# Optimization experiments

Hardware: AMD Instinct MI355X
Metric: run time of the kernel (lower is better)

The kernel has to match this reference:

```python
import jax, jax.numpy as jnp
import numpy as np

N_HEADS = 16


def setup_inputs() -> dict:
    key = jax.random.key(0)
    k1, k2, k3, k4, k5 = jax.random.split(key, 5)
    B, T, C = 2, 2048, 1024
    x = jax.random.normal(k1, (B, T, C), dtype=jnp.float32)
    rotary_cos_sin = jax.random.normal(k2, (T, C // N_HEADS), dtype=jnp.float32)  # unused by forward
    c = jax.random.normal(k3, (B, C), dtype=jnp.float32)  # unused by forward
    # Linear weights, torch convention: y = x @ W.T
    W_qkv = jax.random.normal(k4, (3 * C, C), dtype=jnp.float32) * (1.0 / np.sqrt(C))
    W_out = jax.random.normal(k5, (C, C), dtype=jnp.float32) * (1.0 / np.sqrt(C))
    return {"x": x, "rotary_cos_sin": rotary_cos_sin, "c": c, "W_qkv": W_qkv, "W_out": W_out}


def reference(x, rotary_cos_sin, c, W_qkv, W_out):
    B, T, C = x.shape
    H = N_HEADS
    D = C // H
    # qkv projection (no bias)
    qkv = jnp.einsum('btc,fc->btf', x, W_qkv)          # [B,T,3C]
    q, k, v = jnp.split(qkv, 3, axis=-1)
    q = q.reshape(B, T, H, D)
    k = k.reshape(B, T, H, D)
    v = v.reshape(B, T, H, D)
    # manual attention: full TxT score matrix, as in the original
    att = jnp.einsum('bthd,bshd->bhts', q, k) * (1.0 / jnp.sqrt(jnp.asarray(D, x.dtype)))
    att = jax.nn.softmax(att, axis=-1)
    # attn_dropout / resid_dropout are identity at inference
    y = jnp.einsum('bhts,bshd->bthd', att, v).reshape(B, T, C)
    return jnp.einsum('btc,oc->bto', y, W_out)
```

## Files before the change

kernel.cpp:

```cpp
#include <hip/hip_runtime.h>
#include <hip/hip_bf16.h>

typedef __bf16 bf16;
typedef __attribute__((ext_vector_type(4))) __bf16 bf16x4;
typedef __attribute__((ext_vector_type(8))) __bf16 bf16x8;
typedef __attribute__((ext_vector_type(4))) float f32x4;
typedef __attribute__((ext_vector_type(16))) float f32x16;

#define MFMA16(A, B, C) __builtin_amdgcn_mfma_f32_16x16x32_bf16((A), (B), (C), 0, 0, 0)
#define MFMA32(A, B, C) __builtin_amdgcn_mfma_f32_32x32x16_bf16((A), (B), (C), 0, 0, 0)

union U8 { unsigned w[4]; bf16x8 v; };

__device__ __forceinline__ void gload_lds16(const void* g, void* l) {
    __builtin_amdgcn_global_load_lds(
        (const __attribute__((address_space(1))) void*)g,
        (__attribute__((address_space(3))) void*)l,
        16, 0, 0);
}

__device__ __forceinline__ unsigned pk2(float a, float b) {
    union { bf16 h[2]; unsigned u; } t;
    t.h[0] = (bf16)a; t.h[1] = (bf16)b;
    return t.u;
}

__device__ __forceinline__ unsigned long long tr16(unsigned addr) {
    unsigned long long r;
    asm volatile("ds_read_b64_tr_b16 %0, %1" : "=v"(r) : "v"(addr));
    return r;
}

__global__ __launch_bounds__(256) void cast_f32_bf16(
    const float* __restrict__ in, bf16* __restrict__ out)
{
    const int i = (blockIdx.x * 256 + threadIdx.x) * 8;
    const float4 a = *(const float4*)(in + i);
    const float4 b = *(const float4*)(in + i + 4);
    bf16x8 o;
    o[0] = (bf16)a.x; o[1] = (bf16)a.y; o[2] = (bf16)a.z; o[3] = (bf16)a.w;
    o[4] = (bf16)b.x; o[5] = (bf16)b.y; o[6] = (bf16)b.z; o[7] = (bf16)b.w;
    *(bf16x8*)(out + i) = o;
}

template <typename OutT>
__global__ __launch_bounds__(256) void gemm_bt128(
    const bf16* __restrict__ A, const bf16* __restrict__ B, OutT* __restrict__ C,
    int M, int N, int K)
{
    constexpr int BK = 32;
    __shared__ __align__(16) bf16 sA[128 * BK];
    __shared__ __align__(16) bf16 sB[128 * BK];

    const int tid  = threadIdx.x;
    const int lane = tid & 63;
    const int wave = tid >> 6;
    const int wr   = wave >> 1;
    const int wc   = wave & 1;
    const int bm   = blockIdx.y * 128;
    const int bn   = blockIdx.x * 128;

    f32x4 acc[4][4] = {};

    const size_t ldb = (size_t)K * 2;
    const int srow = wave * 32 + (lane >> 2);
    const int scol = (lane & 3) * 16;
    const char* Ab = (const char*)A + (size_t)(bm + srow) * ldb + scol;
    const char* Bb = (const char*)B + (size_t)(bn + srow) * ldb + scol;
    char* ldsA = (char*)sA + wave * 2048;
    char* ldsB = (char*)sB + wave * 2048;

    const int arow = wr * 64 + (lane & 15);
    const int brow = wc * 64 + (lane & 15);
    const int koff = (lane >> 4) * 8;

    for (int k0 = 0; k0 < K; k0 += BK) {
        __syncthreads();
        const size_t kb = (size_t)k0 * 2;
        gload_lds16(Ab + kb,            ldsA);
        gload_lds16(Ab + kb + 16 * ldb, ldsA + 1024);
        gload_lds16(Bb + kb,            ldsB);
        gload_lds16(Bb + kb + 16 * ldb, ldsB + 1024);
        __syncthreads();

        bf16x8 af[4], bfr[4];
#pragma unroll
        for (int m = 0; m < 4; ++m)
            af[m] = *(const bf16x8*)&sA[(arow + m * 16) * BK + koff];
#pragma unroll
        for (int n = 0; n < 4; ++n)
            bfr[n] = *(const bf16x8*)&sB[(brow + n * 16) * BK + koff];
#pragma unroll
        for (int m = 0; m < 4; ++m)
#pragma unroll
            for (int n = 0; n < 4; ++n)
                acc[m][n] = MFMA16(af[m], bfr[n], acc[m][n]);
    }

    const int crow0 = bm + wr * 64 + (lane >> 4) * 4;
    const int ccol0 = bn + wc * 64 + (lane & 15);
#pragma unroll
    for (int m = 0; m < 4; ++m)
#pragma unroll
        for (int n = 0; n < 4; ++n)
#pragma unroll
            for (int j = 0; j < 4; ++j)
                C[(size_t)(crow0 + m * 16 + j) * N + ccol0 + n * 16] = (OutT)acc[m][n][j];
}

__global__ __launch_bounds__(256, 2) void attn32(
    const bf16* __restrict__ qkv, bf16* __restrict__ y)
{
    constexpr int T = 2048, F = 3072, Cd = 1024;
    constexpr float c1 = 0.18033688011112042f;

    __shared__ __align__(16) bf16 sK[64 * 64];
    __shared__ __align__(16) bf16 sV[64 * 64];

    const int tid = threadIdx.x, lane = tid & 63, wave = tid >> 6;
    const int hi = lane >> 5, q5 = lane & 31;
    const int bh = blockIdx.y, b = bh >> 4, h = bh & 15;
    const bf16* qkvb = qkv + (size_t)b * T * F;
    const int qcol = h * 64, kcol = Cd + h * 64, vcol = 2 * Cd + h * 64;

    const int gq = blockIdx.x * 128 + wave * 32 + q5;
    bf16x8 qf[4];
#pragma unroll
    for (int s = 0; s < 4; ++s)
        qf[s] = *(const bf16x8*)(qkvb + (size_t)gq * F + qcol + s * 16 + hi * 8);

    const int ck0 = (wave * 2 + 0) * 64 + lane, ck1 = ck0 + 64;
    const int kvk0 = ck0 >> 3, d0k0 = ((ck0 & 7) ^ (kvk0 & 7)) << 3;
    const int kvk1 = ck1 >> 3, d0k1 = ((ck1 & 7) ^ (kvk1 & 7)) << 3;
    const int cv0 = ck0, cv1 = ck1;
    const int kvv0 = ((cv0 >> 1) & 3) | (((cv0 >> 5) & 1) << 2) | (((cv0 >> 4) & 1) << 3) | (((cv0 >> 6) & 3) << 4);
    const int dv0  = ((cv0 & 1) << 3) | (((cv0 >> 3) & 1) << 4) | (((cv0 >> 8) & 1) << 5);
    const int kvv1 = ((cv1 >> 1) & 3) | (((cv1 >> 5) & 1) << 2) | (((cv1 >> 4) & 1) << 3) | (((cv1 >> 6) & 3) << 4);
    const int dv1  = ((cv1 & 1) << 3) | (((cv1 >> 3) & 1) << 4) | (((cv1 >> 8) & 1) << 5);

    const char* kq0 = (const char*)qkvb + (size_t)(kvk0 * F + kcol + d0k0) * 2;
    const char* kq1 = (const char*)qkvb + (size_t)(kvk1 * F + kcol + d0k1) * 2;
    const char* vq0 = (const char*)qkvb + (size_t)(kvv0 * F + vcol + dv0) * 2;
    const char* vq1 = (const char*)qkvb + (size_t)(kvv1 * F + vcol + dv1) * 2;
    char* dstK0 = (char*)sK + (wave * 2 + 0) * 1024;
    char* dstK1 = (char*)sK + (wave * 2 + 1) * 1024;
    char* dstV0 = (char*)sV + (wave * 2 + 0) * 1024;
    char* dstV1 = (char*)sV + (wave * 2 + 1) * 1024;

    const unsigned sVoff = (unsigned)(uintptr_t)(__attribute__((address_space(3))) char*)(void*)sV;
    const unsigned trb = sVoff + 8u * (unsigned)lane;

    const unsigned swz = (unsigned)(q5 & 7) << 4;

    f32x16 oacc[2] = {};
    float m_run = -3e38f, l_run = 0.f;

    for (int s0 = 0; s0 < T; s0 += 64) {
        __syncthreads();
        const size_t sb = (size_t)s0 * F * 2;
        gload_lds16(kq0 + sb, dstK0);
        gload_lds16(kq1 + sb, dstK1);
        gload_lds16(vq0 + sb, dstV0);
        gload_lds16(vq1 + sb, dstV1);
        __syncthreads();

        f32x16 sacc[2];
#pragma unroll
        for (int a = 0; a < 2; ++a) {
            f32x16 acc = {};
#pragma unroll
            for (int dsl = 0; dsl < 4; ++dsl) {
                const unsigned cbyte = ((unsigned)(dsl * 32 + hi * 16)) ^ swz;
                bf16x8 kf = *(const bf16x8*)((const char*)sK + (a * 32 + q5) * 128 + cbyte);
                acc = MFMA32(kf, qf[dsl], acc);
            }
            sacc[a] = acc;
        }

        float mt = -3e38f;
#pragma unroll
        for (int a = 0; a < 2; ++a)
#pragma unroll
            for (int r = 0; r < 16; ++r) mt = fmaxf(mt, sacc[a][r]);
        mt = fmaxf(mt, __shfl_xor(mt, 32));
        const float mn = fmaxf(m_run, mt);
        const float al = __builtin_exp2f((m_run - mn) * c1);
        m_run = mn;
        const float mc = mn * c1;

        float rs = 0.f;
        unsigned W[2][4][2];
#pragma unroll
        for (int a = 0; a < 2; ++a)
#pragma unroll
            for (int bb = 0; bb < 4; ++bb) {
                const float p0 = __builtin_exp2f(fmaf(sacc[a][4 * bb + 0], c1, -mc));
                const float p1 = __builtin_exp2f(fmaf(sacc[a][4 * bb + 1], c1, -mc));
                const float p2 = __builtin_exp2f(fmaf(sacc[a][4 * bb + 2], c1, -mc));
                const float p3 = __builtin_exp2f(fmaf(sacc[a][4 * bb + 3], c1, -mc));
                rs += (p0 + p1) + (p2 + p3);
                W[a][bb][0] = pk2(p0, p1);
                W[a][bb][1] = pk2(p2, p3);
            }
        l_run = fmaf(l_run, al, rs);
#pragma unroll
        for (int d = 0; d < 2; ++d)
#pragma unroll
            for (int r = 0; r < 16; ++r) oacc[d][r] *= al;

        unsigned Zz[2][2][2];
#pragma unroll
        for (int a = 0; a < 2; ++a)
#pragma unroll
            for (int c = 0; c < 2; ++c)
#pragma unroll
                for (int w = 0; w < 2; ++w) {
                    const unsigned yv = hi ? W[a][2 * c][w] : W[a][2 * c + 1][w];
                    Zz[a][c][w] = (unsigned)__shfl_xor((int)yv, 32);
                }
        bf16x8 pb[4];
#pragma unroll
        for (int a = 0; a < 2; ++a)
#pragma unroll
            for (int c = 0; c < 2; ++c) {
                U8 u;
                u.w[0] = hi ? Zz[a][c][0] : W[a][2 * c][0];
                u.w[1] = hi ? Zz[a][c][1] : W[a][2 * c][1];
                u.w[2] = hi ? W[a][2 * c + 1][0] : Zz[a][c][0];
                u.w[3] = hi ? W[a][2 * c + 1][1] : Zz[a][c][1];
                pb[2 * a + c] = u.v;
            }

        unsigned long long t0[8], t1[8];
#pragma unroll
        for (int ks = 0; ks < 4; ++ks) {
            t0[2 * ks + 0] = tr16(trb + (unsigned)(ks * 1024));
            t0[2 * ks + 1] = tr16(trb + (unsigned)(ks * 1024 + 512));
        }
#pragma unroll
        for (int ks = 0; ks < 4; ++ks) {
            t1[2 * ks + 0] = tr16(trb + (unsigned)(4096 + ks * 1024));
            t1[2 * ks + 1] = tr16(trb + (unsigned)(4096 + ks * 1024 + 512));
        }
        asm volatile("s_waitcnt lgkmcnt(8)" ::: "memory");
        __builtin_amdgcn_sched_barrier(0);
#pragma unroll
        for (int ks = 0; ks < 4; ++ks) {
            U8 u;
            u.w[0] = (unsigned)t0[2 * ks];     u.w[1] = (unsigned)(t0[2 * ks] >> 32);
            u.w[2] = (unsigned)t0[2 * ks + 1]; u.w[3] = (unsigned)(t0[2 * ks + 1] >> 32);
            oacc[0] = MFMA32(u.v, pb[ks], oacc[0]);
        }
        asm volatile("s_waitcnt lgkmcnt(0)" ::: "memory");
        __builtin_amdgcn_sched_barrier(0);
#pragma unroll
        for (int ks = 0; ks < 4; ++ks) {
            U8 u;
            u.w[0] = (unsigned)t1[2 * ks];     u.w[1] = (unsigned)(t1[2 * ks] >> 32);
            u.w[2] = (unsigned)t1[2 * ks + 1]; u.w[3] = (unsigned)(t1[2 * ks + 1] >> 32);
            oacc[1] = MFMA32(u.v, pb[ks], oacc[1]);
        }
    }

    const float lt = l_run + __shfl_xor(l_run, 32);
    const float inv = 1.f / lt;
    bf16* yrow = y + (size_t)(b * T + gq) * Cd + h * 64;
#pragma unroll
    for (int d = 0; d < 2; ++d)
#pragma unroll
        for (int bb = 0; bb < 4; ++bb) {
            bf16x4 o4;
#pragma unroll
            for (int jj = 0; jj < 4; ++jj)
                o4[jj] = (bf16)(oacc[d][4 * bb + jj] * inv);
            *(bf16x4*)(yrow + d * 32 + 8 * bb + 4 * hi) = o4;
        }
}

extern "C" void kernel_launch(void* const* d_in, const int* in_sizes, int n_in,
                              void* d_out, int out_size, void* d_ws, size_t ws_size,
                              hipStream_t stream) {
    (void)in_sizes; (void)n_in; (void)out_size; (void)ws_size;
    const float* x    = (const float*)d_in[0];
    const float* Wqkv = (const float*)d_in[3];
    const float* Wout = (const float*)d_in[4];
    float* out = (float*)d_out;

    bf16* xb    = (bf16*)d_ws;
    bf16* wqkvb = xb    + (size_t)4096 * 1024;
    bf16* woutb = wqkvb + (size_t)3072 * 1024;
    bf16* qkv   = woutb + (size_t)1024 * 1024;
    bf16* yb    = qkv   + (size_t)4096 * 3072;

    cast_f32_bf16<<<4096 * 1024 / 2048, 256, 0, stream>>>(x, xb);
    cast_f32_bf16<<<3072 * 1024 / 2048, 256, 0, stream>>>(Wqkv, wqkvb);
    cast_f32_bf16<<<1024 * 1024 / 2048, 256, 0, stream>>>(Wout, woutb);

    gemm_bt128<bf16><<<dim3(3072 / 128, 4096 / 128), 256, 0, stream>>>(xb, wqkvb, qkv, 4096, 3072, 1024);
    attn32<<<dim3(2048 / 128, 2 * 16), 256, 0, stream>>>(qkv, yb);
    gemm_bt128<float><<<dim3(1024 / 128, 4096 / 128), 256, 0, stream>>>(yb, woutb, out, 4096, 1024, 1024);
}
```

Baseline: 229.9 us.

## Split attention KV range across two wave groups with LDS merge

The attention block grows to 512 threads, and two groups of four waves each process half of the key/value sequence for the same 128 queries. Partial softmax states are merged through shared memory at the end. The change also adds a lazy rescale that only updates the running max when it grows by more than a threshold, plus s_setprio around the MFMA sections. This targets low occupancy and parallelism in the attention kernel, which previously launched only 512 blocks of 4 waves, at the cost of extra LDS, a final merge step, and a thresholded rescale that could risk overflow on other inputs.

```diff
diff --git a/kernel.cpp b/kernel.cpp
--- a/kernel.cpp
+++ b/kernel.cpp
@@ -108,28 +108,31 @@
                 C[(size_t)(crow0 + m * 16 + j) * N + ccol0 + n * 16] = (OutT)acc[m][n][j];
 }
 
-__global__ __launch_bounds__(256, 2) void attn32(
+__global__ __launch_bounds__(512, 4) void attn32(
     const bf16* __restrict__ qkv, bf16* __restrict__ y)
 {
     constexpr int T = 2048, F = 3072, Cd = 1024;
     constexpr float c1 = 0.18033688011112042f;
 
-    __shared__ __align__(16) bf16 sK[64 * 64];
-    __shared__ __align__(16) bf16 sV[64 * 64];
-
-    const int tid = threadIdx.x, lane = tid & 63, wave = tid >> 6;
+    __shared__ __align__(16) char smem[38912];
+
+    const int tid = threadIdx.x, lane = tid & 63, w = tid >> 6;
+    const int wq = w & 3, grp = w >> 2;
     const int hi = lane >> 5, q5 = lane & 31;
     const int bh = blockIdx.y, b = bh >> 4, h = bh & 15;
     const bf16* qkvb = qkv + (size_t)b * T * F;
     const int qcol = h * 64, kcol = Cd + h * 64, vcol = 2 * Cd + h * 64;
 
-    const int gq = blockIdx.x * 128 + wave * 32 + q5;
+    char* sKg = smem + grp * 8192;
+    char* sVg = smem + 16384 + grp * 8192;
+
+    const int gq = blockIdx.x * 128 + wq * 32 + q5;
     bf16x8 qf[4];
 #pragma unroll
     for (int s = 0; s < 4; ++s)
         qf[s] = *(const bf16x8*)(qkvb + (size_t)gq * F + qcol + s * 16 + hi * 8);
 
-    const int ck0 = (wave * 2 + 0) * 64 + lane, ck1 = ck0 + 64;
+    const int ck0 = (wq * 2 + 0) * 64 + lane, ck1 = ck0 + 64;
     const int kvk0 = ck0 >> 3, d0k0 = ((ck0 & 7) ^ (kvk0 & 7)) << 3;
     const int kvk1 = ck1 >> 3, d0k1 = ((ck1 & 7) ^ (kvk1 & 7)) << 3;
     const int cv0 = ck0, cv1 = ck1;
@@ -138,26 +141,26 @@
     const int kvv1 = ((cv1 >> 1) & 3) | (((cv1 >> 5) & 1) << 2) | (((cv1 >> 4) & 1) << 3) | (((cv1 >> 6) & 3) << 4);
     const int dv1  = ((cv1 & 1) << 3) | (((cv1 >> 3) & 1) << 4) | (((cv1 >> 8) & 1) << 5);
 
-    const char* kq0 = (const char*)qkvb + (size_t)(kvk0 * F + kcol + d0k0) * 2;
-    const char* kq1 = (const char*)qkvb + (size_t)(kvk1 * F + kcol + d0k1) * 2;
-    const char* vq0 = (const char*)qkvb + (size_t)(kvv0 * F + vcol + dv0) * 2;
-    const char* vq1 = (const char*)qkvb + (size_t)(kvv1 * F + vcol + dv1) * 2;
-    char* dstK0 = (char*)sK + (wave * 2 + 0) * 1024;
-    char* dstK1 = (char*)sK + (wave * 2 + 1) * 1024;
-    char* dstV0 = (char*)sV + (wave * 2 + 0) * 1024;
-    char* dstV1 = (char*)sV + (wave * 2 + 1) * 1024;
-
-    const unsigned sVoff = (unsigned)(uintptr_t)(__attribute__((address_space(3))) char*)(void*)sV;
+    const size_t gbase = (size_t)grp * 1024 * F * 2;
+    const char* kq0 = (const char*)qkvb + gbase + (size_t)(kvk0 * F + kcol + d0k0) * 2;
+    const char* kq1 = (const char*)qkvb + gbase + (size_t)(kvk1 * F + kcol + d0k1) * 2;
+    const char* vq0 = (const char*)qkvb + gbase + (size_t)(kvv0 * F + vcol + dv0) * 2;
+    const char* vq1 = (const char*)qkvb + gbase + (size_t)(kvv1 * F + vcol + dv1) * 2;
+    char* dstK0 = sKg + (wq * 2 + 0) * 1024;
+    char* dstK1 = sKg + (wq * 2 + 1) * 1024;
+    char* dstV0 = sVg + (wq * 2 + 0) * 1024;
+    char* dstV1 = sVg + (wq * 2 + 1) * 1024;
+
+    const unsigned sVoff = (unsigned)(uintptr_t)(__attribute__((address_space(3))) char*)(void*)sVg;
     const unsigned trb = sVoff + 8u * (unsigned)lane;
-
     const unsigned swz = (unsigned)(q5 & 7) << 4;
 
     f32x16 oacc[2] = {};
     float m_run = -3e38f, l_run = 0.f;
 
-    for (int s0 = 0; s0 < T; s0 += 64) {
+    for (int it = 0; it < 16; ++it) {
         __syncthreads();
-        const size_t sb = (size_t)s0 * F * 2;
+        const size_t sb = (size_t)it * 64 * F * 2;
         gload_lds16(kq0 + sb, dstK0);
         gload_lds16(kq1 + sb, dstK1);
         gload_lds16(vq0 + sb, dstV0);
@@ -165,17 +168,19 @@
         __syncthreads();
 
         f32x16 sacc[2];
+        __builtin_amdgcn_s_setprio(1);
 #pragma unroll
         for (int a = 0; a < 2; ++a) {
             f32x16 acc = {};
 #pragma unroll
             for (int dsl = 0; dsl < 4; ++dsl) {
                 const unsigned cbyte = ((unsigned)(dsl * 32 + hi * 16)) ^ swz;
-                bf16x8 kf = *(const bf16x8*)((const char*)sK + (a * 32 + q5) * 128 + cbyte);
+                bf16x8 kf = *(const bf16x8*)(sKg + (a * 32 + q5) * 128 + cbyte);
                 acc = MFMA32(kf, qf[dsl], acc);
             }
             sacc[a] = acc;
         }
+        __builtin_amdgcn_s_setprio(0);
 
         float mt = -3e38f;
 #pragma unroll
@@ -183,10 +188,17 @@
 #pragma unroll
             for (int r = 0; r < 16; ++r) mt = fmaxf(mt, sacc[a][r]);
         mt = fmaxf(mt, __shfl_xor(mt, 32));
-        const float mn = fmaxf(m_run, mt);
-        const float al = __builtin_exp2f((m_run - mn) * c1);
-        m_run = mn;
-        const float mc = mn * c1;
+        if (__any(mt > m_run + 64.0f)) {
+            const float mn = fmaxf(m_run, mt);
+            const float al = __builtin_exp2f((m_run - mn) * c1);
+            m_run = mn;
+            l_run *= al;
+#pragma unroll
+            for (int d = 0; d < 2; ++d)
+#pragma unroll
+                for (int r = 0; r < 16; ++r) oacc[d][r] *= al;
+        }
+        const float mc = m_run * c1;
 
         float rs = 0.f;
         unsigned W[2][4][2];
@@ -202,11 +214,7 @@
                 W[a][bb][0] = pk2(p0, p1);
                 W[a][bb][1] = pk2(p2, p3);
             }
-        l_run = fmaf(l_run, al, rs);
-#pragma unroll
-        for (int d = 0; d < 2; ++d)
-#pragma unroll
-            for (int r = 0; r < 16; ++r) oacc[d][r] *= al;
+        l_run += rs;
 
         unsigned Zz[2][2][2];
 #pragma unroll
@@ -214,9 +222,9 @@
 #pragma unroll
             for (int c = 0; c < 2; ++c)
 #pragma unroll
-                for (int w = 0; w < 2; ++w) {
-                    const unsigned yv = hi ? W[a][2 * c][w] : W[a][2 * c + 1][w];
-                    Zz[a][c][w] = (unsigned)__shfl_xor((int)yv, 32);
+                for (int ww = 0; ww < 2; ++ww) {
+                    const unsigned yv = hi ? W[a][2 * c][ww] : W[a][2 * c + 1][ww];
+                    Zz[a][c][ww] = (unsigned)__shfl_xor((int)yv, 32);
                 }
         bf16x8 pb[4];
 #pragma unroll
@@ -244,6 +252,7 @@
         }
         asm volatile("s_waitcnt lgkmcnt(8)" ::: "memory");
         __builtin_amdgcn_sched_barrier(0);
+        __builtin_amdgcn_s_setprio(1);
 #pragma unroll
         for (int ks = 0; ks < 4; ++ks) {
             U8 u;
@@ -251,8 +260,10 @@
             u.w[2] = (unsigned)t0[2 * ks + 1]; u.w[3] = (unsigned)(t0[2 * ks + 1] >> 32);
             oacc[0] = MFMA32(u.v, pb[ks], oacc[0]);
         }
+        __builtin_amdgcn_s_setprio(0);
         asm volatile("s_waitcnt lgkmcnt(0)" ::: "memory");
         __builtin_amdgcn_sched_barrier(0);
+        __builtin_amdgcn_s_setprio(1);
 #pragma unroll
         for (int ks = 0; ks < 4; ++ks) {
             U8 u;
@@ -260,21 +271,50 @@
             u.w[2] = (unsigned)t1[2 * ks + 1]; u.w[3] = (unsigned)(t1[2 * ks + 1] >> 32);
             oacc[1] = MFMA32(u.v, pb[ks], oacc[1]);
         }
+        __builtin_amdgcn_s_setprio(0);
     }
 
-    const float lt = l_run + __shfl_xor(l_run, 32);
-    const float inv = 1.f / lt;
-    bf16* yrow = y + (size_t)(b * T + gq) * Cd + h * 64;
-#pragma unroll
-    for (int d = 0; d < 2; ++d)
-#pragma unroll
-        for (int bb = 0; bb < 4; ++bb) {
-            bf16x4 o4;
-#pragma unroll
-            for (int jj = 0; jj < 4; ++jj)
-                o4[jj] = (bf16)(oacc[d][4 * bb + jj] * inv);
-            *(bf16x4*)(yrow + d * 32 + 8 * bb + 4 * hi) = o4;
-        }
+    __syncthreads();
+    float* Obuf  = (float*)smem;
+    float* mlbuf = (float*)(smem + 36864);
+    if (grp == 1) {
+        float* po = Obuf + (wq * 64 + lane) * 36;
+#pragma unroll
+        for (int d5 = 0; d5 < 2; ++d5)
+#pragma unroll
+            for (int j = 0; j < 4; ++j) {
+                f32x4 t;
+                t[0] = oacc[d5][4 * j + 0]; t[1] = oacc[d5][4 * j + 1];
+                t[2] = oacc[d5][4 * j + 2]; t[3] = oacc[d5][4 * j + 3];
+                *(f32x4*)(po + d5 * 16 + 4 * j) = t;
+            }
+        mlbuf[(wq * 64 + lane) * 2 + 0] = m_run;
+        mlbuf[(wq * 64 + lane) * 2 + 1] = l_run;
+    }
+    __syncthreads();
+    if (grp == 0) {
+        const float mB = mlbuf[(wq * 64 + lane) * 2 + 0];
+        const float lB = mlbuf[(wq * 64 + lane) * 2 + 1];
+        const float m  = fmaxf(m_run, mB);
+        const float fA = __builtin_exp2f((m_run - m) * c1);
+        const float fB = __builtin_exp2f((mB - m) * c1);
+        const float lh = l_run * fA + lB * fB;
+        const float lt = lh + __shfl_xor(lh, 32);
+        const float inv = 1.f / lt;
+        const float* po = Obuf + (wq * 64 + lane) * 36;
+        bf16* yrow = y + (size_t)(b * T + gq) * Cd + h * 64;
+#pragma unroll
+        for (int d5 = 0; d5 < 2; ++d5)
+#pragma unroll
+            for (int bb = 0; bb < 4; ++bb) {
+                const f32x4 ob = *(const f32x4*)(po + d5 * 16 + 4 * bb);
+                bf16x4 o4;
+#pragma unroll
+                for (int jj = 0; jj < 4; ++jj)
+                    o4[jj] = (bf16)((oacc[d5][4 * bb + jj] * fA + ob[jj] * fB) * inv);
+                *(bf16x4*)(yrow + d5 * 32 + 8 * bb + 4 * hi) = o4;
+            }
+    }
 }
 
 extern "C" void kernel_launch(void* const* d_in, const int* in_sizes, int n_in,
@@ -297,6 +337,6 @@
     cast_f32_bf16<<<1024 * 1024 / 2048, 256, 0, stream>>>(Wout, woutb);
 
     gemm_bt128<bf16><<<dim3(3072 / 128, 4096 / 128), 256, 0, stream>>>(xb, wqkvb, qkv, 4096, 3072, 1024);
-    attn32<<<dim3(2048 / 128, 2 * 16), 256, 0, stream>>>(qkv, yb);
+    attn32<<<dim3(2048 / 128, 2 * 16), 512, 0, stream>>>(qkv, yb);
     gemm_bt128<float><<<dim3(1024 / 128, 4096 / 128), 256, 0, stream>>>(yb, woutb, out, 4096, 1024, 1024);
 }
```

Result: no change. 226.4 us (-1.5%).
